# Optimization experiments

Measured on AMD Instinct MI355X. Metric: run time of the kernel, lower is better.

The kernel has to match this reference:

```python
import jax, jax.numpy as jnp
import numpy as np

NUM_USERS = 100000
NUM_ITEMS = 50000
EMBED_DIM = 64
N_LAYERS = 3
NUM_EDGES = 3276800  # avg user degree 32
BATCH = 16384


def setup_inputs() -> dict:
    key = jax.random.key(0)
    k0, k1, k2, k3, k4, k5 = jax.random.split(key, 6)
    rows = jax.random.randint(k0, (NUM_EDGES,), 0, NUM_USERS, dtype=jnp.int32)
    cols = jax.random.randint(k1, (NUM_EDGES,), 0, NUM_ITEMS, dtype=jnp.int32)
    user_table = jax.random.normal(k2, (NUM_USERS, EMBED_DIM), dtype=jnp.float32) * 0.1
    item_table = jax.random.normal(k3, (NUM_ITEMS, EMBED_DIM), dtype=jnp.float32) * 0.1
    user_indices = jax.random.randint(k4, (BATCH,), 0, NUM_USERS, dtype=jnp.int32)
    item_indices = jax.random.randint(k5, (BATCH,), 0, NUM_ITEMS, dtype=jnp.int32)
    return {
        "user_table": user_table,
        "item_table": item_table,
        "rows": rows,
        "cols": cols,
        "user_indices": user_indices,
        "item_indices": item_indices,
    }


def reference(user_table, item_table, rows, cols, user_indices, item_indices):
    # D^-1 A row-normalization of the binary bipartite adjacency:
    # normalized edge value for edge (u, i) is 1 / deg(u) (0 if isolated).
    ones = jnp.ones(rows.shape, dtype=user_table.dtype)
    deg = jax.ops.segment_sum(ones, rows, num_segments=NUM_USERS)
    inv_deg = jnp.where(deg > 0, 1.0 / deg, 0.0)
    vals = inv_deg[rows]  # [E]

    u = user_table  # [U, D] (unused by propagation in the original too)
    it = item_table  # [I, D]
    for _ in range(N_LAYERS):
        # u = A @ it  (SpMM via gather + segment-sum over destination users)
        u = jax.ops.segment_sum(vals[:, None] * it[cols], rows, num_segments=NUM_USERS)
        # it = A^T @ u
        it = jax.ops.segment_sum(vals[:, None] * u[rows], cols, num_segments=NUM_ITEMS)

    scores = jnp.sum(u[user_indices] * it[item_indices], axis=-1)  # [B]
    return jax.nn.sigmoid(scores)
```

## Files before the change

### kernel.cpp

```cpp
#include <hip/hip_runtime.h>
#include <math.h>

#define NUM_USERS 100000
#define NUM_ITEMS 50000
#define EMBED     64
#define NUM_EDGES 3276800
#define BATCH     16384
#define CAP       12800
#define NBUCK     391
#define P1_EDGES  8192
#define P1_THREADS 512
#define P2_THREADS 1024
#define CVT_GROUPS (NUM_ITEMS * 8)
#define CVT_BLOCKS ((CVT_GROUPS + P1_THREADS - 1) / P1_THREADS)

typedef _Float16 half8 __attribute__((ext_vector_type(8)));

union H8 { half8 v; int i[4]; };

__device__ __forceinline__ half8 slot_reduce(half8 acc) {
    H8 a; a.v = acc;
    H8 o;
    #pragma unroll
    for (int j = 0; j < 4; ++j) o.i[j] = __shfl_xor(a.i[j], 8, 64);
    a.v += o.v;
    #pragma unroll
    for (int j = 0; j < 4; ++j) o.i[j] = __shfl_xor(a.i[j], 16, 64);
    a.v += o.v;
    #pragma unroll
    for (int j = 0; j < 4; ++j) o.i[j] = __shfl_xor(a.i[j], 32, 64);
    a.v += o.v;
    return a.v;
}

__device__ __forceinline__ unsigned scan_incl_512(unsigned val, unsigned* swv, int t) {
    unsigned x = val;
    #pragma unroll
    for (int o = 1; o < 64; o <<= 1) {
        unsigned y = __shfl_up(x, o, 64);
        if ((t & 63) >= o) x += y;
    }
    if ((t & 63) == 63) swv[t >> 6] = x;
    __syncthreads();
    unsigned base = 0;
    int w = t >> 6;
    #pragma unroll
    for (int i = 0; i < 7; ++i)
        base += (i < w) ? swv[i] : 0;
    return x + base;
}

__global__ void __launch_bounds__(P1_THREADS)
build_kernel(const int* __restrict__ rows, const int* __restrict__ cols,
             const float* __restrict__ itab, _Float16* __restrict__ it16,
             _Float16* __restrict__ w16,
             int* __restrict__ ucur, int* __restrict__ icur,
             int* __restrict__ rec_u, int* __restrict__ rec_i) {
    __shared__ int hu[400], hi[400], gu[400], gi[400];
    __shared__ int lbase[400], lcur[400];
    __shared__ unsigned scp[512];
    __shared__ unsigned swv[8];
    __shared__ int recbuf[P1_EDGES];
    int t = threadIdx.x;

    if (blockIdx.x >= 400) {
        int b = blockIdx.x - 400;
        if (b < CVT_BLOCKS) {
            int i = b * P1_THREADS + t;
            if (i < CVT_GROUPS) {
                const float4* p = (const float4*)itab + 2 * i;
                float4 a = p[0], c = p[1];
                half8 o;
                o[0] = (_Float16)a.x; o[1] = (_Float16)a.y; o[2] = (_Float16)a.z; o[3] = (_Float16)a.w;
                o[4] = (_Float16)c.x; o[5] = (_Float16)c.y; o[6] = (_Float16)c.z; o[7] = (_Float16)c.w;
                ((half8*)it16)[i] = o;
            }
        } else {
            if (t < 64) w16[(long long)NUM_USERS * EMBED + t] = (_Float16)0.f;
            else if (t < 128) it16[(long long)NUM_ITEMS * EMBED + (t - 64)] = (_Float16)0.f;
        }
        return;
    }

    long long e0 = (long long)blockIdx.x * P1_EDGES;
    int er[16], ec[16];
    #pragma unroll
    for (int q = 0; q < 16; ++q) {
        er[q] = rows[e0 + t + q * P1_THREADS];
        ec[q] = cols[e0 + t + q * P1_THREADS];
    }

    for (int i = t; i < 400; i += P1_THREADS) { hu[i] = 0; hi[i] = 0; }
    __syncthreads();
    #pragma unroll
    for (int q = 0; q < 16; ++q) {
        atomicAdd(&hu[er[q] >> 8], 1);
        atomicAdd(&hi[ec[q] >> 7], 1);
    }
    __syncthreads();
    for (int i = t; i < 400; i += P1_THREADS) {
        int vr = (hu[i] + 15) & ~15;
        gu[i] = vr ? atomicAdd(&ucur[i], vr) : 0;
        vr = (hi[i] + 15) & ~15;
        gi[i] = vr ? atomicAdd(&icur[i], vr) : 0;
    }

    {
        unsigned hv = (t < 400) ? (unsigned)hu[t] : 0u;
        unsigned val = (((hv + 15u) & ~15u) << 16) | hv;
        unsigned incl = scan_incl_512(val, swv, t);
        scp[t] = incl;
        if (t < 400) { lbase[t] = (int)(incl & 0xffffu) - (int)hv; lcur[t] = 0; }
    }
    __syncthreads();
    #pragma unroll
    for (int q = 0; q < 16; ++q) {
        int b = er[q] >> 8;
        int p = lbase[b] + atomicAdd(&lcur[b], 1);
        recbuf[p] = (ec[q] << 8) | (er[q] & 255);
    }
    __syncthreads();
    {
        int total = (int)(scp[511] >> 16);
        for (int o4 = t * 4; o4 < total; o4 += P1_THREADS * 4) {
            int lo = 0, hi_ = 399;
            while (lo < hi_) { int mid = (lo + hi_) >> 1; if ((int)(scp[mid] >> 16) > o4) hi_ = mid; else lo = mid + 1; }
            int b = lo;
            int v = hu[b];
            int vr = (v + 15) & ~15;
            int j = o4 - ((int)(scp[b] >> 16) - vr);
            int gpos = gu[b] + j;
            if (gpos + 3 < CAP) {
                int4 val;
                val.x = (j + 0 < v) ? recbuf[lbase[b] + j + 0] : -1;
                val.y = (j + 1 < v) ? recbuf[lbase[b] + j + 1] : -1;
                val.z = (j + 2 < v) ? recbuf[lbase[b] + j + 2] : -1;
                val.w = (j + 3 < v) ? recbuf[lbase[b] + j + 3] : -1;
                *(int4*)(rec_u + (long long)b * CAP + gpos) = val;
            } else {
                for (int k = 0; k < 4; ++k)
                    if (gpos + k < CAP)
                        rec_u[(long long)b * CAP + gpos + k] = (j + k < v) ? recbuf[lbase[b] + j + k] : -1;
            }
        }
    }
    __syncthreads();

    {
        unsigned hv = (t < 400) ? (unsigned)hi[t] : 0u;
        unsigned val = (((hv + 15u) & ~15u) << 16) | hv;
        unsigned incl = scan_incl_512(val, swv, t);
        scp[t] = incl;
        if (t < 400) { lbase[t] = (int)(incl & 0xffffu) - (int)hv; lcur[t] = 0; }
    }
    __syncthreads();
    #pragma unroll
    for (int q = 0; q < 16; ++q) {
        int b = ec[q] >> 7;
        int p = lbase[b] + atomicAdd(&lcur[b], 1);
        recbuf[p] = (er[q] << 7) | (ec[q] & 127);
    }
    __syncthreads();
    {
        int total = (int)(scp[511] >> 16);
        for (int o4 = t * 4; o4 < total; o4 += P1_THREADS * 4) {
            int lo = 0, hi_ = 399;
            while (lo < hi_) { int mid = (lo + hi_) >> 1; if ((int)(scp[mid] >> 16) > o4) hi_ = mid; else lo = mid + 1; }
            int b = lo;
            int v = hi[b];
            int vr = (v + 15) & ~15;
            int j = o4 - ((int)(scp[b] >> 16) - vr);
            int gpos = gi[b] + j;
            if (gpos + 3 < CAP) {
                int4 val;
                val.x = (j + 0 < v) ? recbuf[lbase[b] + j + 0] : -1;
                val.y = (j + 1 < v) ? recbuf[lbase[b] + j + 1] : -1;
                val.z = (j + 2 < v) ? recbuf[lbase[b] + j + 2] : -1;
                val.w = (j + 3 < v) ? recbuf[lbase[b] + j + 3] : -1;
                *(int4*)(rec_i + (long long)b * CAP + gpos) = val;
            } else {
                for (int k = 0; k < 4; ++k)
                    if (gpos + k < CAP)
                        rec_i[(long long)b * CAP + gpos + k] = (j + k < v) ? recbuf[lbase[b] + j + k] : -1;
            }
        }
    }
}

template <int VBITS>
__device__ __forceinline__ void pass2_body(int* __restrict__ rec, const int* __restrict__ cur,
                                           int* __restrict__ deg, int* __restrict__ off,
                                           float* __restrict__ inv32, int ncap, int b, int sentinel,
                                           int* buf, int* h, int* ex, int* cnt, unsigned* swv) {
    const int V = 1 << VBITS, M = V - 1;
    int t = threadIdx.x;
    long long s = (long long)b * CAP;
    int n = cur[b]; if (n > CAP) n = CAP;
    int nv = (n + 3) >> 2;
    const int4* rec4 = (const int4*)(rec + s);
    for (int i = t; i < nv; i += P2_THREADS) {
        int4 v4 = rec4[i];
        buf[4 * i + 0] = v4.x; buf[4 * i + 1] = v4.y;
        buf[4 * i + 2] = v4.z; buf[4 * i + 3] = v4.w;
    }
    if (t < V) { h[t] = 0; cnt[t] = 0; }
    __syncthreads();
    for (int i = t; i < n; i += P2_THREADS) {
        int r = buf[i];
        if (r != -1) atomicAdd(&h[r & M], 1);
    }
    __syncthreads();
    unsigned ph = 0, x = 0;
    {
        unsigned hv = (t < V) ? (unsigned)h[t] : 0u;
        ph = (hv + 15u) & ~15u;
        x = ph;
        #pragma unroll
        for (int o = 1; o < 64; o <<= 1) {
            unsigned y = __shfl_up(x, o, 64);
            if ((t & 63) >= o) x += y;
        }
        if ((t & 63) == 63 && t < V) swv[t >> 6] = x;
    }
    __syncthreads();
    if (t < V) {
        unsigned base = 0;
        int w = t >> 6;
        #pragma unroll
        for (int i = 0; i < (V >> 6); ++i)
            base += (i < w) ? swv[i] : 0;
        int pb = (int)(x + base - ph);
        ex[t] = pb;
        int id = b * V + t;
        if (id < ncap) {
            int v = h[t];
            deg[id] = v;
            off[id] = (int)(s + pb);
            if (inv32) inv32[id] = v ? 1.0f / (float)v : 0.0f;
        }
        for (int j = h[t]; j < (int)ph && pb + j < CAP; ++j) rec[s + pb + j] = sentinel;
    }
    __syncthreads();
    for (int i = t; i < n; i += P2_THREADS) {
        int r = buf[i];
        if (r == -1) continue;
        int k = r & M;
        int rnk = atomicAdd(&cnt[k], 1);
        int p = ex[k] + rnk;
        if (p < CAP)
            rec[s + p] = (int)((((unsigned)r) >> VBITS) << 7);
    }
}

__global__ void __launch_bounds__(P2_THREADS)
pass2_kernel(int* __restrict__ rec_u, const int* __restrict__ ucur,
             int* __restrict__ udeg, int* __restrict__ uoff, float* __restrict__ inv32,
             int* __restrict__ rec_i, const int* __restrict__ icur,
             int* __restrict__ ideg, int* __restrict__ ioff) {
    __shared__ int buf[CAP];
    __shared__ int h[256], ex[256], cnt[256];
    __shared__ unsigned swv[8];
    if (blockIdx.x < NBUCK)
        pass2_body<8>(rec_u, ucur, udeg, uoff, inv32, NUM_USERS, blockIdx.x,
                      NUM_ITEMS << 7, buf, h, ex, cnt, swv);
    else
        pass2_body<7>(rec_i, icur, ideg, ioff, (float*)nullptr, NUM_ITEMS,
                      blockIdx.x - NBUCK, NUM_USERS << 7, buf, h, ex, cnt, swv);
}

__global__ void gather_u(const int* __restrict__ uoff, const int* __restrict__ udeg,
                         const int* __restrict__ csr_boff, const float* __restrict__ inv32,
                         const _Float16* __restrict__ it, _Float16* __restrict__ w) {
    int row = blockIdx.x * 4 + (threadIdx.x >> 6);
    if (row >= NUM_USERS) return;
    int lane = threadIdx.x & 63;
    int slot = lane >> 3;
    int h    = lane & 7;
    int start = uoff[row];
    int pend = start + ((udeg[row] + 15) & ~15);
    const char* itb = (const char*)it;
    unsigned hoff = (unsigned)(h << 4);
    half8 acc = {};
    int k = start;
    for (; k + 32 <= pend; k += 32) {
        int4 o = *(const int4*)(csr_boff + k + slot * 4);
        half8 x0 = *(const half8*)(itb + ((unsigned)o.x + hoff));
        half8 x1 = *(const half8*)(itb + ((unsigned)o.y + hoff));
        half8 x2 = *(const half8*)(itb + ((unsigned)o.z + hoff));
        half8 x3 = *(const half8*)(itb + ((unsigned)o.w + hoff));
        acc += (x0 + x1) + (x2 + x3);
    }
    if (k < pend) {
        int2 o2 = *(const int2*)(csr_boff + k + slot * 2);
        half8 x0 = *(const half8*)(itb + ((unsigned)o2.x + hoff));
        half8 x1 = *(const half8*)(itb + ((unsigned)o2.y + hoff));
        acc += x0 + x1;
    }
    half8 r = slot_reduce(acc);
    if (lane < 8) {
        float v = inv32[row];
        float v2 = v * v;
        half8 ow;
        #pragma unroll
        for (int j = 0; j < 8; ++j) ow[j] = (_Float16)((float)r[j] * v2);
        *(half8*)(w + (long long)row * EMBED + (lane << 3)) = ow;
    }
}

__global__ void gather_it(const int* __restrict__ ioff, const int* __restrict__ ideg,
                          const int* __restrict__ csc_boff,
                          const _Float16* __restrict__ w, _Float16* __restrict__ it) {
    int col = blockIdx.x * 4 + (threadIdx.x >> 6);
    if (col >= NUM_ITEMS) return;
    int lane = threadIdx.x & 63;
    int slot = lane >> 3;
    int h    = lane & 7;
    int start = ioff[col];
    int pend = start + ((ideg[col] + 15) & ~15);
    const char* wb = (const char*)w;
    unsigned hoff = (unsigned)(h << 4);
    half8 acc = {};
    int k = start;
    for (; k + 32 <= pend; k += 32) {
        int4 o = *(const int4*)(csc_boff + k + slot * 4);
        half8 x0 = *(const half8*)(wb + ((unsigned)o.x + hoff));
        half8 x1 = *(const half8*)(wb + ((unsigned)o.y + hoff));
        half8 x2 = *(const half8*)(wb + ((unsigned)o.z + hoff));
        half8 x3 = *(const half8*)(wb + ((unsigned)o.w + hoff));
        acc += (x0 + x1) + (x2 + x3);
    }
    if (k < pend) {
        int2 o2 = *(const int2*)(csc_boff + k + slot * 2);
        half8 x0 = *(const half8*)(wb + ((unsigned)o2.x + hoff));
        half8 x1 = *(const half8*)(wb + ((unsigned)o2.y + hoff));
        acc += x0 + x1;
    }
    half8 r = slot_reduce(acc);
    if (lane < 8)
        *(half8*)(it + (long long)col * EMBED + (lane << 3)) = r;
}

__global__ void batch_score(const int* __restrict__ ioff, const int* __restrict__ ideg,
                            const int* __restrict__ csc_boff, const _Float16* __restrict__ w,
                            const int* __restrict__ udeg,
                            const int* __restrict__ uidx, const int* __restrict__ iidx,
                            float* __restrict__ out) {
    int b = blockIdx.x * 4 + (threadIdx.x >> 6);
    if (b >= BATCH) return;
    int lane = threadIdx.x & 63;
    int col = iidx[b];
    int slot = lane >> 3;
    int h    = lane & 7;
    int start = ioff[col];
    int pend = start + ((ideg[col] + 15) & ~15);
    const char* wb = (const char*)w;
    unsigned hoff = (unsigned)(h << 4);
    half8 acc = {};
    int k = start;
    for (; k + 32 <= pend; k += 32) {
        int4 o = *(const int4*)(csc_boff + k + slot * 4);
        half8 x0 = *(const half8*)(wb + ((unsigned)o.x + hoff));
        half8 x1 = *(const half8*)(wb + ((unsigned)o.y + hoff));
        half8 x2 = *(const half8*)(wb + ((unsigned)o.z + hoff));
        half8 x3 = *(const half8*)(wb + ((unsigned)o.w + hoff));
        acc += (x0 + x1) + (x2 + x3);
    }
    if (k < pend) {
        int2 o2 = *(const int2*)(csc_boff + k + slot * 2);
        half8 x0 = *(const half8*)(wb + ((unsigned)o2.x + hoff));
        half8 x1 = *(const half8*)(wb + ((unsigned)o2.y + hoff));
        acc += x0 + x1;
    }
    half8 r = slot_reduce(acc);
    int ui = uidx[b];
    half8 wv = *(const half8*)(w + (long long)ui * EMBED + (h << 3));
    float p = 0.f;
    #pragma unroll
    for (int j = 0; j < 8; ++j) p += (float)r[j] * (float)wv[j];
    p += __shfl_xor(p, 1, 64);
    p += __shfl_xor(p, 2, 64);
    p += __shfl_xor(p, 4, 64);
    if (lane == 0) {
        float s = p * (float)udeg[ui];
        out[b] = 1.0f / (1.0f + expf(-s));
    }
}

extern "C" void kernel_launch(void* const* d_in, const int* in_sizes, int n_in,
                              void* d_out, int out_size, void* d_ws, size_t ws_size,
                              hipStream_t stream) {
    const float* item_table = (const float*)d_in[1];
    const int*   rows       = (const int*)d_in[2];
    const int*   cols       = (const int*)d_in[3];
    const int*   uidx       = (const int*)d_in[4];
    const int*   iidx       = (const int*)d_in[5];
    float* out = (float*)d_out;

    char* base = (char*)d_ws;
    int*   udeg  = (int*)(base + 0);
    int*   ideg  = (int*)(base +   400000);
    int*   uoff  = (int*)(base +   600000);
    int*   ioff  = (int*)(base +  1000000);
    float* inv32 = (float*)(base + 1200000);
    int*   ucur  = (int*)(base +  1600000);
    int*   icur  = (int*)(base +  1601600);
    int*   rec_u = (int*)(base +  1720320);
    int*   rec_i = (int*)(base + 22200320);
    _Float16* w16  = (_Float16*)(base + 42680320);
    _Float16* it16 = (_Float16*)(base + 55480448);

    (void)hipMemsetAsync(ucur, 0, 3200, stream);

    build_kernel<<<400 + CVT_BLOCKS + 1, P1_THREADS, 0, stream>>>(
        rows, cols, item_table, it16, w16, ucur, icur, rec_u, rec_i);
    pass2_kernel<<<NBUCK * 2, P2_THREADS, 0, stream>>>(rec_u, ucur, udeg, uoff, inv32,
                                                       rec_i, icur, ideg, ioff);

    const int ublocks = (NUM_USERS + 3) / 4;
    const int iblocks = (NUM_ITEMS + 3) / 4;
    for (int l = 0; l < 3; ++l) {
        gather_u<<<ublocks, 256, 0, stream>>>(uoff, udeg, rec_u, inv32, it16, w16);
        if (l < 2)
            gather_it<<<iblocks, 256, 0, stream>>>(ioff, ideg, rec_i, w16, it16);
    }
    batch_score<<<BATCH / 4, 256, 0, stream>>>(ioff, ideg, rec_i, w16, udeg,
                                               uidx, iidx, out);
}
```

Baseline: 397.6 us.

## Fuse propagation layers into one persistent kernel with grid barriers

Replaces the six gather launches and the scoring launch with a single persistent kernel of 1024 blocks. Blocks grid-stride over rows and synchronise between layers with an atomic-counter grid barrier, whose counter is zeroed by the existing memset. This removes per-launch overhead and tail gaps between the dependent phases. In exchange it requires all 1024 blocks to be co-resident, otherwise the barrier deadlocks, and it adds barrier spin latency plus possibly lower occupancy than the original launches.

```diff
diff --git a/kernel.cpp b/kernel.cpp
--- a/kernel.cpp
+++ b/kernel.cpp
@@ -11,6 +11,7 @@
 #define P1_EDGES  8192
 #define P1_THREADS 512
 #define P2_THREADS 1024
+#define PROP_BLOCKS 1024
 #define CVT_GROUPS (NUM_ITEMS * 8)
 #define CVT_BLOCKS ((CVT_GROUPS + P1_THREADS - 1) / P1_THREADS)
 
@@ -48,6 +49,18 @@
     for (int i = 0; i < 7; ++i)
         base += (i < w) ? swv[i] : 0;
     return x + base;
+}
+
+__device__ __forceinline__ void grid_barrier(unsigned* bar, unsigned target) {
+    __syncthreads();
+    if (threadIdx.x == 0) {
+        __threadfence();
+        __hip_atomic_fetch_add(bar, 1u, __ATOMIC_RELEASE, __HIP_MEMORY_SCOPE_AGENT);
+        while (__hip_atomic_load(bar, __ATOMIC_ACQUIRE, __HIP_MEMORY_SCOPE_AGENT) < target)
+            __builtin_amdgcn_s_sleep(8);
+        __threadfence();
+    }
+    __syncthreads();
 }
 
 __global__ void __launch_bounds__(P1_THREADS)
@@ -268,10 +281,11 @@
                       blockIdx.x - NBUCK, NUM_USERS << 7, buf, h, ex, cnt, swv);
 }
 
-__global__ void gather_u(const int* __restrict__ uoff, const int* __restrict__ udeg,
-                         const int* __restrict__ csr_boff, const float* __restrict__ inv32,
-                         const _Float16* __restrict__ it, _Float16* __restrict__ w) {
-    int row = blockIdx.x * 4 + (threadIdx.x >> 6);
+__device__ __forceinline__ void gather_u_body(int vb,
+        const int* __restrict__ uoff, const int* __restrict__ udeg,
+        const int* __restrict__ csr_boff, const float* __restrict__ inv32,
+        const _Float16* __restrict__ it, _Float16* __restrict__ w) {
+    int row = vb * 4 + (threadIdx.x >> 6);
     if (row >= NUM_USERS) return;
     int lane = threadIdx.x & 63;
     int slot = lane >> 3;
@@ -307,10 +321,11 @@
     }
 }
 
-__global__ void gather_it(const int* __restrict__ ioff, const int* __restrict__ ideg,
-                          const int* __restrict__ csc_boff,
-                          const _Float16* __restrict__ w, _Float16* __restrict__ it) {
-    int col = blockIdx.x * 4 + (threadIdx.x >> 6);
+__device__ __forceinline__ void gather_it_body(int vb,
+        const int* __restrict__ ioff, const int* __restrict__ ideg,
+        const int* __restrict__ csc_boff,
+        const _Float16* __restrict__ w, _Float16* __restrict__ it) {
+    int col = vb * 4 + (threadIdx.x >> 6);
     if (col >= NUM_ITEMS) return;
     int lane = threadIdx.x & 63;
     int slot = lane >> 3;
@@ -340,12 +355,13 @@
         *(half8*)(it + (long long)col * EMBED + (lane << 3)) = r;
 }
 
-__global__ void batch_score(const int* __restrict__ ioff, const int* __restrict__ ideg,
-                            const int* __restrict__ csc_boff, const _Float16* __restrict__ w,
-                            const int* __restrict__ udeg,
-                            const int* __restrict__ uidx, const int* __restrict__ iidx,
-                            float* __restrict__ out) {
-    int b = blockIdx.x * 4 + (threadIdx.x >> 6);
+__device__ __forceinline__ void batch_score_body(int vb,
+        const int* __restrict__ ioff, const int* __restrict__ ideg,
+        const int* __restrict__ csc_boff, const _Float16* __restrict__ w,
+        const int* __restrict__ udeg,
+        const int* __restrict__ uidx, const int* __restrict__ iidx,
+        float* __restrict__ out) {
+    int b = vb * 4 + (threadIdx.x >> 6);
     if (b >= BATCH) return;
     int lane = threadIdx.x & 63;
     int col = iidx[b];
@@ -386,6 +402,33 @@
     }
 }
 
+__global__ void __launch_bounds__(256, 4)
+propagate(const int* __restrict__ uoff, const int* __restrict__ udeg,
+          const int* __restrict__ rec_u, const float* __restrict__ inv32,
+          const int* __restrict__ ioff, const int* __restrict__ ideg,
+          const int* __restrict__ rec_i,
+          _Float16* __restrict__ w, _Float16* __restrict__ it,
+          const int* __restrict__ uidx, const int* __restrict__ iidx,
+          float* __restrict__ out, unsigned* __restrict__ bar) {
+    const unsigned NB = gridDim.x;
+    const int UV = (NUM_USERS + 3) / 4;
+    const int IV = (NUM_ITEMS + 3) / 4;
+    unsigned phase = 0;
+    #pragma unroll 1
+    for (int l = 0; l < 3; ++l) {
+        for (int vb = blockIdx.x; vb < UV; vb += NB)
+            gather_u_body(vb, uoff, udeg, rec_u, inv32, it, w);
+        grid_barrier(bar, ++phase * NB);
+        if (l < 2) {
+            for (int vb = blockIdx.x; vb < IV; vb += NB)
+                gather_it_body(vb, ioff, ideg, rec_i, w, it);
+            grid_barrier(bar, ++phase * NB);
+        }
+    }
+    for (int vb = blockIdx.x; vb < BATCH / 4; vb += NB)
+        batch_score_body(vb, ioff, ideg, rec_i, w, udeg, uidx, iidx, out);
+}
+
 extern "C" void kernel_launch(void* const* d_in, const int* in_sizes, int n_in,
                               void* d_out, int out_size, void* d_ws, size_t ws_size,
                               hipStream_t stream) {
@@ -404,25 +447,20 @@
     float* inv32 = (float*)(base + 1200000);
     int*   ucur  = (int*)(base +  1600000);
     int*   icur  = (int*)(base +  1601600);
+    unsigned* bar = (unsigned*)(base + 1603200);
     int*   rec_u = (int*)(base +  1720320);
     int*   rec_i = (int*)(base + 22200320);
     _Float16* w16  = (_Float16*)(base + 42680320);
     _Float16* it16 = (_Float16*)(base + 55480448);
 
-    (void)hipMemsetAsync(ucur, 0, 3200, stream);
+    (void)hipMemsetAsync(ucur, 0, 3264, stream);
 
     build_kernel<<<400 + CVT_BLOCKS + 1, P1_THREADS, 0, stream>>>(
         rows, cols, item_table, it16, w16, ucur, icur, rec_u, rec_i);
     pass2_kernel<<<NBUCK * 2, P2_THREADS, 0, stream>>>(rec_u, ucur, udeg, uoff, inv32,
                                                        rec_i, icur, ideg, ioff);
 
-    const int ublocks = (NUM_USERS + 3) / 4;
-    const int iblocks = (NUM_ITEMS + 3) / 4;
-    for (int l = 0; l < 3; ++l) {
-        gather_u<<<ublocks, 256, 0, stream>>>(uoff, udeg, rec_u, inv32, it16, w16);
-        if (l < 2)
-            gather_it<<<iblocks, 256, 0, stream>>>(ioff, ideg, rec_i, w16, it16);
-    }
-    batch_score<<<BATCH / 4, 256, 0, stream>>>(ioff, ideg, rec_i, w16, udeg,
-                                               uidx, iidx, out);
-}
+    propagate<<<PROP_BLOCKS, 256, 0, stream>>>(uoff, udeg, rec_u, inv32,
+                                               ioff, ideg, rec_i, w16, it16,
+                                               uidx, iidx, out, bar);
+}
```

Result: slower. 1.346 ms (+238.5%).
